# Kernel tuning notes

Hardware: AMD Instinct MI355X
Metric: run time of the kernel (lower is better)

The kernel has to match this reference:

```python
import jax, jax.numpy as jnp
import numpy as np

B, T = 65536, 256
E = H = 5

def setup_inputs() -> dict:
    key = jax.random.key(0)
    ks = jax.random.split(key, 8)
    return {
        "x": jax.random.randint(ks[0], (B, T), 0, 2),
        "emb": jax.random.normal(ks[1], (2, E), jnp.float32),
        "W_ih": jax.random.normal(ks[2], (4 * H, E), jnp.float32) * 0.3,
        "W_hh": jax.random.normal(ks[3], (4 * H, H), jnp.float32) * 0.3,
        "b_ih": jax.random.normal(ks[4], (4 * H,), jnp.float32) * 0.1,
        "b_hh": jax.random.normal(ks[5], (4 * H,), jnp.float32) * 0.1,
        "W_lin": jax.random.normal(ks[6], (2, H), jnp.float32) * 0.3,
        "b_lin": jax.random.normal(ks[7], (2,), jnp.float32) * 0.1,
    }

def reference(x, emb, W_ih, W_hh, b_ih, b_hh, W_lin, b_lin):
    # Embedding lookup: [B, T] int -> [B, T, E]
    xe = emb[x]
    # Precompute input contributions to all 4 gates for every timestep: [B, T, 4H]
    gx = jnp.einsum("bte,ge->btg", xe, W_ih) + (b_ih + b_hh)
    Whh_T = W_hh.T  # [H, 4H]

    def step(carry, gx_t):
        h, c = carry  # each [B, H]
        gates = gx_t + h @ Whh_T  # [B, 4H]
        i, f, g, o = jnp.split(gates, 4, axis=-1)  # PyTorch gate order i,f,g,o
        i = jax.nn.sigmoid(i)
        f = jax.nn.sigmoid(f)
        g = jnp.tanh(g)
        o = jax.nn.sigmoid(o)
        c = f * c + i * g
        h = o * jnp.tanh(c)
        return (h, c), None

    h0 = jnp.zeros((x.shape[0], H), xe.dtype)
    c0 = jnp.zeros((x.shape[0], H), xe.dtype)
    # scan over time (axis 1 -> move to leading axis)
    (h_last, _), _ = jax.lax.scan(step, (h0, c0), jnp.swapaxes(gx, 0, 1))
    # Final-step linear head: [B, H] -> [B, 2]
    return h_last @ W_lin.T + b_lin
```

## Files before the change

### kernel.cpp

```cpp
#include <hip/hip_runtime.h>


typedef float v2f __attribute__((ext_vector_type(2)));

constexpr int TT = 256;
constexpr int EE = 5;
constexpr int HH = 5;
constexpr int GG = 20;
constexpr int GP = 10;

__device__ __forceinline__ float fexp2(float v) { return __builtin_amdgcn_exp2f(v); }
__device__ __forceinline__ float frcp(float v)  { return __builtin_amdgcn_rcpf(v); }

__global__ __launch_bounds__(256, 1) void lstm_fused(
    const int* __restrict__ x,
    const float* __restrict__ emb,
    const float* __restrict__ W_ih,
    const float* __restrict__ W_hh,
    const float* __restrict__ b_ih,
    const float* __restrict__ b_hh,
    const float* __restrict__ W_lin,
    const float* __restrict__ b_lin,
    float* __restrict__ out)
{
    const int b = blockIdx.x * blockDim.x + threadIdx.x;

    const float NL2E  = -1.4426950408889634f;
    const float T2L2E =  2.8853900817779268f;

    float base_s[GG], delta_s[GG];
#pragma unroll
    for (int g = 0; g < GG; ++g) {
        float g0 = b_ih[g] + b_hh[g];
        float g1 = g0;
#pragma unroll
        for (int e = 0; e < EE; ++e) {
            float w = W_ih[g * EE + e];
            g0 = fmaf(w, emb[e], g0);
            g1 = fmaf(w, emb[EE + e], g1);
        }
        float s = (g >= 10 && g < 15) ? T2L2E : NL2E;
        base_s[g]  = s * g0;
        delta_s[g] = s * (g1 - g0);
    }

    v2f basepk[GP], deltapk[GP];
    v2f wpk[HH][GP];
#pragma unroll
    for (int p = 0; p < GP; ++p) {
        float b0 = base_s[2*p],  b1 = base_s[2*p+1];
        float d0 = delta_s[2*p], d1 = delta_s[2*p+1];
        asm volatile("" : "+v"(b0), "+v"(b1), "+v"(d0), "+v"(d1));
        basepk[p][0] = b0;  basepk[p][1] = b1;
        deltapk[p][0] = d0; deltapk[p][1] = d1;
        float s0 = (2*p   >= 10 && 2*p   < 15) ? T2L2E : NL2E;
        float s1 = (2*p+1 >= 10 && 2*p+1 < 15) ? T2L2E : NL2E;
#pragma unroll
        for (int j = 0; j < HH; ++j) {
            float w0 = s0 * W_hh[(2*p)   * HH + j];
            float w1 = s1 * W_hh[(2*p+1) * HH + j];
            asm volatile("" : "+v"(w0), "+v"(w1));
            wpk[j][p][0] = w0; wpk[j][p][1] = w1;
        }
    }

    float h[HH] = {0.f, 0.f, 0.f, 0.f, 0.f};
    float c[HH] = {0.f, 0.f, 0.f, 0.f, 0.f};

    auto step = [&](int xt) {
        const float xtf = (float)xt;
        v2f xpk; xpk[0] = xtf; xpk[1] = xtf;
        v2f g[GP];
#pragma unroll
        for (int p = 0; p < GP; ++p)
            g[p] = __builtin_elementwise_fma(xpk, deltapk[p], basepk[p]);
#pragma unroll
        for (int j = 0; j < HH; ++j) {
            v2f hj; hj[0] = h[j]; hj[1] = h[j];
#pragma unroll
            for (int p = 0; p < GP; ++p)
                g[p] = __builtin_elementwise_fma(wpk[j][p], hj, g[p]);
        }
#pragma unroll
        for (int j = 0; j < HH; ++j) {
            float gi = g[(j)      >> 1][(j)      & 1];
            float gf = g[(5 + j)  >> 1][(5 + j)  & 1];
            float gg = g[(10 + j) >> 1][(10 + j) & 1];
            float go = g[(15 + j) >> 1][(15 + j) & 1];
            float iv = frcp(1.0f + fexp2(gi));
            float fv = frcp(1.0f + fexp2(gf));
            float gv = fmaf(-2.0f, frcp(1.0f + fexp2(gg)), 1.0f);
            float ov = frcp(1.0f + fexp2(go));
            float cn = fmaf(fv, c[j], iv * gv);
            c[j] = cn;
            float tc = fmaf(-2.0f, frcp(1.0f + fexp2(cn * T2L2E)), 1.0f);
            h[j] = ov * tc;
        }
    };

    const int4* xr = reinterpret_cast<const int4*>(x + (size_t)b * TT);
    int4 cur = xr[0];
#pragma unroll 1
    for (int it = 0; it < TT / 4 - 1; ++it) {
        int4 nxt = xr[it + 1];
        step(cur.x);
        step(cur.y);
        step(cur.z);
        step(cur.w);
        cur = nxt;
    }
    step(cur.x);
    step(cur.y);
    step(cur.z);
    step(cur.w);

    float o0 = b_lin[0], o1 = b_lin[1];
#pragma unroll
    for (int j = 0; j < HH; ++j) {
        o0 = fmaf(W_lin[j],      h[j], o0);
        o1 = fmaf(W_lin[HH + j], h[j], o1);
    }
    reinterpret_cast<float2*>(out)[b] = make_float2(o0, o1);
}

extern "C" void kernel_launch(void* const* d_in, const int* in_sizes, int n_in,
                              void* d_out, int out_size, void* d_ws, size_t ws_size,
                              hipStream_t stream) {
    const int* x        = (const int*)d_in[0];
    const float* emb    = (const float*)d_in[1];
    const float* W_ih   = (const float*)d_in[2];
    const float* W_hh   = (const float*)d_in[3];
    const float* b_ih   = (const float*)d_in[4];
    const float* b_hh   = (const float*)d_in[5];
    const float* W_lin  = (const float*)d_in[6];
    const float* b_lin  = (const float*)d_in[7];
    float* out          = (float*)d_out;

    const int B = in_sizes[0] / TT;
    const int block = 256;
    const int grid = B / block;

    lstm_fused<<<grid, block, 0, stream>>>(x, emb, W_ih, W_hh, b_ih, b_hh,
                                           W_lin, b_lin, out);
}
```

Before: 108.0 us.

## Merge LSTM gate reciprocals algebraically and share reciprocals across hidden-unit pairs

Rewrites the gate nonlinearities so each hidden unit's cell update folds the sigmoid and tanh denominators into a single division, keeping the cell state pre-scaled by 2*log2(e). It then shares one reciprocal between pairs of hidden units by inverting the product of their denominators. This cuts the transcendental rcp count per step from 25 to 6 at the cost of extra multiplies. The products of several (1+exp) terms can overflow for large gate magnitudes, which risks inf/NaN where the old form saturated cleanly.

```diff
diff --git a/kernel.cpp b/kernel.cpp
--- a/kernel.cpp
+++ b/kernel.cpp
@@ -64,8 +64,8 @@
         }
     }
 
-    float h[HH] = {0.f, 0.f, 0.f, 0.f, 0.f};
-    float c[HH] = {0.f, 0.f, 0.f, 0.f, 0.f};
+    float h[HH]    = {0.f, 0.f, 0.f, 0.f, 0.f};
+    float chat[HH] = {0.f, 0.f, 0.f, 0.f, 0.f};
 
     auto step = [&](int xt) {
         const float xtf = (float)xt;
@@ -81,20 +81,46 @@
             for (int p = 0; p < GP; ++p)
                 g[p] = __builtin_elementwise_fma(wpk[j][p], hj, g[p]);
         }
+        auto G = [&](int idx) -> float { return g[idx >> 1][idx & 1]; };
+
+        float N[HH], D[HH];
 #pragma unroll
         for (int j = 0; j < HH; ++j) {
-            float gi = g[(j)      >> 1][(j)      & 1];
-            float gf = g[(5 + j)  >> 1][(5 + j)  & 1];
-            float gg = g[(10 + j) >> 1][(10 + j) & 1];
-            float go = g[(15 + j) >> 1][(15 + j) & 1];
-            float iv = frcp(1.0f + fexp2(gi));
-            float fv = frcp(1.0f + fexp2(gf));
-            float gv = fmaf(-2.0f, frcp(1.0f + fexp2(gg)), 1.0f);
-            float ov = frcp(1.0f + fexp2(go));
-            float cn = fmaf(fv, c[j], iv * gv);
-            c[j] = cn;
-            float tc = fmaf(-2.0f, frcp(1.0f + fexp2(cn * T2L2E)), 1.0f);
-            h[j] = ov * tc;
+            float Ei = fexp2(G(j));
+            float Ef = fexp2(G(5 + j));
+            float Eg = fexp2(G(10 + j));
+            float Ai = 1.0f + Ei, Af = 1.0f + Ef, Ag = 1.0f + Eg;
+            float P  = Ai * Ag;
+            D[j] = P * Af;
+            float t = fmaf(T2L2E, Eg, -T2L2E);
+            N[j] = fmaf(chat[j], P, t * Af);
+        }
+        {
+            float R01 = frcp(D[0] * D[1]);
+            chat[0] = (N[0] * D[1]) * R01;
+            chat[1] = (N[1] * D[0]) * R01;
+            float R23 = frcp(D[2] * D[3]);
+            chat[2] = (N[2] * D[3]) * R23;
+            chat[3] = (N[3] * D[2]) * R23;
+            chat[4] = N[4] * frcp(D[4]);
+        }
+
+        float T2[HH], D2[HH];
+#pragma unroll
+        for (int j = 0; j < HH; ++j) {
+            float Eo = fexp2(G(15 + j));
+            float Ec = fexp2(chat[j]);
+            D2[j] = (1.0f + Eo) * (1.0f + Ec);
+            T2[j] = Ec - 1.0f;
+        }
+        {
+            float R01 = frcp(D2[0] * D2[1]);
+            h[0] = (T2[0] * D2[1]) * R01;
+            h[1] = (T2[1] * D2[0]) * R01;
+            float R23 = frcp(D2[2] * D2[3]);
+            h[2] = (T2[2] * D2[3]) * R23;
+            h[3] = (T2[3] * D2[2]) * R23;
+            h[4] = T2[4] * frcp(D2[4]);
         }
     };
 
```

Measured after the change: 95.58 us. 1.13x faster.
